# Performance work log

Hardware: AMD Instinct MI355X
Metric: run time of the kernel (lower is better)

The kernel has to match this reference:

```python
import jax, jax.numpy as jnp
import numpy as np

TEMPERATURE = 0.07
C_MARGIN = 0.5
T_MARGIN = 1.0
GAMMA = 2.0
ALPHA = 0.25
SMOOTHING = 0.1
W_CONTRASTIVE = 0.1
W_TRIPLET = 0.1
W_FOCAL = 0.4
W_LABEL_SMOOTH = 0.4


def setup_inputs() -> dict:
    key = jax.random.key(0)
    k1, k2, k3 = jax.random.split(key, 3)
    B, C, D = 2048, 1000, 512
    pred = jax.random.normal(k1, (B, C), dtype=jnp.float32)
    target = jax.random.randint(k2, (B,), 0, C, dtype=jnp.int64)
    features = jax.random.normal(k3, (B, D), dtype=jnp.float32)
    return {"pred": pred, "target": target, "features": features}


def _safe_cdist(f):
    # Euclidean pairwise distance with zero-grad at zero distance (matches torch.cdist on diagonal).
    r = jnp.sum(f * f, axis=1)
    d2 = jnp.maximum(r[:, None] - 2.0 * (f @ f.T) + r[None, :], 0.0)
    pos = d2 > 0
    return jnp.sqrt(jnp.where(pos, d2, 1.0)) * pos


def _contrastive(features, labels):
    f = features / jnp.linalg.norm(features, axis=1, keepdims=True)
    sim = f @ f.T  # [B, B]
    lm = (labels[:, None] == labels[None, :]).astype(sim.dtype)
    pos = sim * lm
    pos_loss = -jnp.log(jnp.exp(pos / TEMPERATURE) + 1e-8)
    neg = sim * (1.0 - lm)
    neg_loss = jnp.maximum(C_MARGIN - neg, 0.0)
    return pos_loss.mean() + neg_loss.mean()


def _triplet(features, labels):
    B = features.shape[0]
    d = _safe_cdist(features)  # [B, B]
    lm = (labels[:, None] == labels[None, :]).astype(d.dtype)
    pm, nm = lm, 1.0 - lm

    def body(acc, args):
        di, pmi, nmi = args  # [B], [B], [B]
        # sum over (p, n): relu(d_ip - d_in + margin), masked
        contrib = jnp.sum(
            jnp.maximum(di[:, None] - di[None, :] + T_MARGIN, 0.0)
            * pmi[:, None] * nmi[None, :]
        )
        return acc + contrib, None

    loss, _ = jax.lax.scan(body, jnp.float32(0.0), (d, pm, nm))
    return loss / (B + 1e-8)


def _focal(pred, target):
    logp = jax.nn.log_softmax(pred, axis=1)
    ce = -jnp.take_along_axis(logp, target[:, None], axis=1)[:, 0]
    pt = jnp.exp(-ce)
    return (ALPHA * (1.0 - pt) ** GAMMA * ce).mean()


def _label_smoothing(pred, target):
    C = pred.shape[1]
    off = SMOOTHING / (C - 1)
    logp = jax.nn.log_softmax(pred, axis=1)
    # smooth target: off everywhere, (1 - smoothing) at target index
    tgt_logp = jnp.take_along_axis(logp, target[:, None], axis=1)[:, 0]
    loss = -(off * logp.sum(axis=1) + ((1.0 - SMOOTHING) - off) * tgt_logp)
    return loss.mean()


def reference(pred, target, features):
    lc = _contrastive(features, target)
    lt = _triplet(features, target)
    lf = _focal(pred, target)
    ls = _label_smoothing(pred, target)
    total = (W_CONTRASTIVE * lc + W_TRIPLET * lt
             + W_FOCAL * lf + W_LABEL_SMOOTH * ls)
    return jnp.stack([lc, lt, lf, ls, total])
```

## Files before the change

### kernel.cpp

```cpp
#include <hip/hip_runtime.h>
#include <hip/hip_bf16.h>
#include <math.h>

typedef __attribute__((ext_vector_type(8))) short bf16x8;
typedef __attribute__((ext_vector_type(4))) float f32x4;

static constexpr float TEMP_INV  = 1.0f / 0.07f;
static constexpr float C_MARGIN  = 0.5f;
static constexpr float T_MARGIN  = 1.0f;
static constexpr float ALPHA     = 0.25f;
static constexpr float SMOOTHING = 0.1f;

__device__ __forceinline__ void gload_lds16(const void* g, void* l) {
    __builtin_amdgcn_global_load_lds(
        (const __attribute__((address_space(1))) void*)g,
        (__attribute__((address_space(3))) void*)l,
        16, 0, 0);
}

__device__ __forceinline__ unsigned short f2bf(float x) {
    __hip_bfloat16 h = __float2bfloat16(x);
    return *reinterpret_cast<unsigned short*>(&h);
}
__device__ __forceinline__ float bf2f(unsigned short u) {
    union { unsigned int u32; float f; } U;
    U.u32 = ((unsigned int)u) << 16;
    return U.f;
}

__global__ __launch_bounds__(256) void prep_kernel(
    const float* __restrict__ F, unsigned short* __restrict__ Fb,
    float* __restrict__ diag, float* __restrict__ inv_norm, int D) {
    const int row  = blockIdx.x * 4 + (threadIdx.x >> 6);
    const int lane = threadIdx.x & 63;
    const float4* Fr  = (const float4*)(F + (size_t)row * D);
    ushort4*      Fbr = (ushort4*)(Fb + (size_t)row * D);
    const int n4 = D >> 2;
    float s = 0.0f;
    for (int idx = lane; idx < n4; idx += 64) {
        float4 v = Fr[idx];
        s += v.x * v.x + v.y * v.y + v.z * v.z + v.w * v.w;
        ushort4 o;
        o.x = f2bf(v.x); o.y = f2bf(v.y); o.z = f2bf(v.z); o.w = f2bf(v.w);
        Fbr[idx] = o;
    }
#pragma unroll
    for (int off = 32; off > 0; off >>= 1) s += __shfl_down(s, off, 64);
    if (lane == 0) { diag[row] = s; inv_norm[row] = 1.0f / sqrtf(s); }
}

__global__ __launch_bounds__(256) void gram_ce_kernel(
    const unsigned short* __restrict__ Fb, unsigned short* __restrict__ Gb,
    const float* __restrict__ pred, const int* __restrict__ target,
    float* __restrict__ partialCE, int B, int D, int C, float off_const,
    int tilesX) {
    __shared__ unsigned short As[128 * 32];
    __shared__ unsigned short Bs[128 * 32];
    __shared__ float red[12];

    const int nTiles = tilesX * tilesX;
    const int tid = threadIdx.x;
    const int lane = tid & 63, wid = tid >> 6;

    if (blockIdx.x < nTiles) {
        const int rowBase = (blockIdx.x / tilesX) * 128;
        const int colBase = (blockIdx.x % tilesX) * 128;
        const int w = wid, l = lane;
        const int wr = (w >> 1) * 64;
        const int wc = (w & 1) * 64;
        const int half = l >> 4;
        const int rr   = l & 15;

        const unsigned short* FA = Fb + (size_t)rowBase * D;
        const unsigned short* FB = Fb + (size_t)colBase * D;

        f32x4 acc[4][4];
#pragma unroll
        for (int m = 0; m < 4; ++m)
#pragma unroll
            for (int n = 0; n < 4; ++n) acc[m][n] = (f32x4){0.f, 0.f, 0.f, 0.f};

        for (int k0 = 0; k0 < D; k0 += 32) {
#pragma unroll
            for (int c = 0; c < 2; ++c) {
                const int chunk = c * 256 + w * 64 + l;
                const int r2 = chunk >> 2;
                const int ss = (l & 3) ^ (r2 & 3);
                const size_t eoff = (size_t)r2 * D + k0 + ss * 8;
                gload_lds16(FA + eoff, &As[(c * 256 + w * 64) * 8]);
                gload_lds16(FB + eoff, &Bs[(c * 256 + w * 64) * 8]);
            }
            __syncthreads();
            bf16x8 af[4], bfv[4];
#pragma unroll
            for (int f = 0; f < 4; ++f) {
                const int ar = wr + f * 16 + rr;
                af[f]  = *(const bf16x8*)(&As[ar * 32 + ((half ^ (ar & 3)) * 8)]);
                const int br = wc + f * 16 + rr;
                bfv[f] = *(const bf16x8*)(&Bs[br * 32 + ((half ^ (br & 3)) * 8)]);
            }
#pragma unroll
            for (int m = 0; m < 4; ++m)
#pragma unroll
                for (int n = 0; n < 4; ++n)
                    acc[m][n] = __builtin_amdgcn_mfma_f32_16x16x32_bf16(
                        af[m], bfv[n], acc[m][n], 0, 0, 0);
            __syncthreads();
        }
#pragma unroll
        for (int m = 0; m < 4; ++m) {
            const int i0 = rowBase + wr + m * 16 + half * 4;
#pragma unroll
            for (int n = 0; n < 4; ++n) {
                const int j = colBase + wc + n * 16 + rr;
#pragma unroll
                for (int r = 0; r < 4; ++r)
                    Gb[(size_t)(i0 + r) * B + j] = f2bf(acc[m][n][r]);
            }
        }
    } else {
        const int i = blockIdx.x - nTiles;
        const float* prow = pred + (size_t)i * C;
        const float tlogit = prow[target[i]];
        const int Cv = C >> 2;

        float m = -1e30f, s = 0.0f, sp = 0.0f;
        for (int idx = tid; idx < Cv; idx += 256) {
            float4 v = ((const float4*)prow)[idx];
            float mv = fmaxf(fmaxf(v.x, v.y), fmaxf(v.z, v.w));
            if (mv > m) { s *= expf(m - mv); m = mv; }
            s += expf(v.x - m) + expf(v.y - m) + expf(v.z - m) + expf(v.w - m);
            sp += v.x + v.y + v.z + v.w;
        }
        for (int j = Cv * 4 + tid; j < C; j += 256) {
            float v = prow[j];
            if (v > m) { s *= expf(m - v); m = v; }
            s += expf(v - m);
            sp += v;
        }
#pragma unroll
        for (int off = 32; off > 0; off >>= 1) {
            float mo = __shfl_down(m, off, 64);
            float so = __shfl_down(s, off, 64);
            sp += __shfl_down(sp, off, 64);
            float mx = fmaxf(m, mo);
            s = s * expf(m - mx) + so * expf(mo - mx);
            m = mx;
        }
        if (lane == 0) { red[wid] = m; red[4 + wid] = s; red[8 + wid] = sp; }
        __syncthreads();
        if (tid == 0) {
            float mm = red[0], ss = red[4], spT = red[8];
#pragma unroll
            for (int q = 1; q < 4; ++q) {
                float mo = red[q], so = red[4 + q];
                float mn = fmaxf(mm, mo);
                ss = ss * expf(mm - mn) + so * expf(mo - mn);
                mm = mn;
                spT += red[8 + q];
            }
            float lse = mm + logf(ss);
            float tl  = tlogit - lse;
            float ce  = -tl;
            float pt  = expf(tl);
            float omp = 1.0f - pt;
            float focal = ALPHA * omp * omp * ce;
            float sumlogp = spT - (float)C * lse;
            float lsv = -(off_const * sumlogp + ((1.0f - SMOOTHING) - off_const) * tl);
            partialCE[(size_t)i * 2]     = focal;
            partialCE[(size_t)i * 2 + 1] = lsv;
        }
    }
}

__global__ __launch_bounds__(256) void row_loss_kernel(
    const unsigned short* __restrict__ Gb, const float* __restrict__ diag,
    const float* __restrict__ inv_norm, const int* __restrict__ labels,
    float* __restrict__ partial, int B) {
    __shared__ float p_d[256];
    __shared__ float red[12];
    __shared__ int p_cnt;
    const int tid = threadIdx.x;
    const int i = blockIdx.x;
    if (tid == 0) p_cnt = 0;
    __syncthreads();

    const int   li     = labels[i];
    const float ri     = diag[i];
    const float inv_ni = inv_norm[i];
    const int   j0     = tid * 8;

    union { uint4 u; unsigned short s[8]; } GV;
    GV.u = *(const uint4*)(Gb + (size_t)i * B + j0);
    int lab[8];
    *(int4*)&lab[0] = *(const int4*)(labels + j0);
    *(int4*)&lab[4] = *(const int4*)(labels + j0 + 4);
    float dg[8], ivn[8];
    *(float4*)&dg[0]  = *(const float4*)(diag + j0);
    *(float4*)&dg[4]  = *(const float4*)(diag + j0 + 4);
    *(float4*)&ivn[0] = *(const float4*)(inv_norm + j0);
    *(float4*)&ivn[4] = *(const float4*)(inv_norm + j0 + 4);

    float pos = 0.0f, neg = 0.0f;
    float d8[8];
    int mmask = 0;
#pragma unroll
    for (int e = 0; e < 8; ++e) {
        const int j = j0 + e;
        const float g = bf2f(GV.s[e]);
        float sim = g * inv_ni * ivn[e];
        const float d2 = ri - 2.0f * g + dg[e];
        float d = (d2 > 0.0f) ? sqrtf(d2) : 0.0f;
        if (j == i) { sim = 1.0f; d = 0.0f; }
        d8[e] = d;
        if (lab[e] == li) {
            pos += -logf(expf(sim * TEMP_INV) + 1e-8f);
            neg += C_MARGIN;
            mmask |= (1 << e);
            int slot = atomicAdd(&p_cnt, 1);
            if (slot < 256) p_d[slot] = d;
        } else {
            neg += fmaxf(C_MARGIN - sim, 0.0f);
        }
    }
    __syncthreads();
    const int cnt = (p_cnt < 256) ? p_cnt : 256;
    float trip = 0.0f;
    for (int p = 0; p < cnt; ++p) {
        const float dp = p_d[p] + T_MARGIN;
#pragma unroll
        for (int e = 0; e < 8; ++e)
            if (!(mmask & (1 << e))) trip += fmaxf(dp - d8[e], 0.0f);
    }

    float r0 = pos, r1 = neg, r2 = trip;
#pragma unroll
    for (int off = 32; off > 0; off >>= 1) {
        r0 += __shfl_down(r0, off, 64);
        r1 += __shfl_down(r1, off, 64);
        r2 += __shfl_down(r2, off, 64);
    }
    const int lane = tid & 63, wid = tid >> 6;
    if (lane == 0) { red[wid] = r0; red[4 + wid] = r1; red[8 + wid] = r2; }
    __syncthreads();
    if (tid == 0) {
        float4 o;
        o.x = red[0] + red[1] + red[2] + red[3];
        o.y = red[4] + red[5] + red[6] + red[7];
        o.z = red[8] + red[9] + red[10] + red[11];
        o.w = 0.0f;
        *(float4*)(partial + (size_t)i * 4) = o;
    }
}

__global__ __launch_bounds__(256) void reduce_kernel(
    const float* __restrict__ partialT, const float* __restrict__ partialCE,
    float* __restrict__ out, int B) {
    __shared__ float red[4][5];
    const int tid = threadIdx.x;
    float s[5] = {0.f, 0.f, 0.f, 0.f, 0.f};
    for (int r = tid; r < B; r += 256) {
        float4 v = *(const float4*)(partialT + (size_t)r * 4);
        s[0] += v.x; s[1] += v.y; s[2] += v.z;
    }
    for (int t = tid; t < (B * 2) / 4; t += 256) {
        float4 v = *(const float4*)(partialCE + (size_t)t * 4);
        s[3] += v.x + v.z; s[4] += v.y + v.w;
    }
#pragma unroll
    for (int off = 32; off > 0; off >>= 1) {
#pragma unroll
        for (int k = 0; k < 5; ++k) s[k] += __shfl_down(s[k], off, 64);
    }
    const int lane = tid & 63, wid = tid >> 6;
    if (lane == 0) {
#pragma unroll
        for (int k = 0; k < 5; ++k) red[wid][k] = s[k];
    }
    __syncthreads();
    if (tid == 0) {
        float t[5];
#pragma unroll
        for (int k = 0; k < 5; ++k)
            t[k] = red[0][k] + red[1][k] + red[2][k] + red[3][k];
        double invB2 = 1.0 / ((double)B * (double)B);
        float lc = (float)(((double)t[0] + (double)t[1]) * invB2);
        float lt = (float)((double)t[2] / ((double)B + 1e-8));
        float lf = t[3] / (float)B;
        float ls = t[4] / (float)B;
        out[0] = lc;
        out[1] = lt;
        out[2] = lf;
        out[3] = ls;
        out[4] = 0.1f * lc + 0.1f * lt + 0.4f * lf + 0.4f * ls;
    }
}

extern "C" void kernel_launch(void* const* d_in, const int* in_sizes, int n_in,
                              void* d_out, int out_size, void* d_ws, size_t ws_size,
                              hipStream_t stream) {
    const float* pred     = (const float*)d_in[0];
    const int*   target   = (const int*)d_in[1];
    const float* features = (const float*)d_in[2];
    const int B = in_sizes[1];
    const int C = in_sizes[0] / B;
    const int D = in_sizes[2] / B;
    float* out = (float*)d_out;
    const int tilesX = B / 128;
    const int nTiles = tilesX * tilesX;

    float* partial   = (float*)d_ws;
    float* partialCE = partial + (size_t)B * 4;
    float* diag      = partialCE + (size_t)B * 2;
    float* inv_norm  = diag + B;
    unsigned short* Fb = (unsigned short*)(inv_norm + B);
    unsigned short* Gb = Fb + (size_t)B * D;

    prep_kernel<<<B / 4, 256, 0, stream>>>(features, Fb, diag, inv_norm, D);

    float off_const = SMOOTHING / (float)(C - 1);
    gram_ce_kernel<<<nTiles + B, 256, 0, stream>>>(
        Fb, Gb, pred, target, partialCE, B, D, C, off_const, tilesX);

    row_loss_kernel<<<B, 256, 0, stream>>>(Gb, diag, inv_norm, target,
                                           partial, B);

    reduce_kernel<<<1, 256, 0, stream>>>(partial, partialCE, out, B);
}
```

Baseline: 38.15 us.

## Exploit Gram symmetry to compute upper tiles only; process several rows per block

The Gram kernel now computes only tiles on or above the diagonal and writes each off-diagonal tile twice, once as is and once transposed, which roughly halves the MFMA work. The row-loss kernel handles four rows per block and loads the per-column labels, norms and diag values once for all four. The transposed stores are strided 8-byte writes, which may coalesce poorly. Early-returning blocks still take launch slots.

Measured after the change: 44.39 us. 16.3% more time.

```diff
diff --git a/kernel.cpp b/kernel.cpp
--- a/kernel.cpp
+++ b/kernel.cpp
@@ -10,6 +10,7 @@
 static constexpr float T_MARGIN  = 1.0f;
 static constexpr float ALPHA     = 0.25f;
 static constexpr float SMOOTHING = 0.1f;
+static constexpr int   RPB       = 4;
 
 __device__ __forceinline__ void gload_lds16(const void* g, void* l) {
     __builtin_amdgcn_global_load_lds(
@@ -63,8 +64,11 @@
     const int lane = tid & 63, wid = tid >> 6;
 
     if (blockIdx.x < nTiles) {
-        const int rowBase = (blockIdx.x / tilesX) * 128;
-        const int colBase = (blockIdx.x % tilesX) * 128;
+        const int ti = blockIdx.x / tilesX;
+        const int tj = blockIdx.x % tilesX;
+        if (tj < ti) return;
+        const int rowBase = ti * 128;
+        const int colBase = tj * 128;
         const int w = wid, l = lane;
         const int wr = (w >> 1) * 64;
         const int wc = (w & 1) * 64;
@@ -116,6 +120,22 @@
 #pragma unroll
                 for (int r = 0; r < 4; ++r)
                     Gb[(size_t)(i0 + r) * B + j] = f2bf(acc[m][n][r]);
+            }
+        }
+        if (ti != tj) {
+#pragma unroll
+            for (int m = 0; m < 4; ++m) {
+                const int i0 = rowBase + wr + m * 16 + half * 4;
+#pragma unroll
+                for (int n = 0; n < 4; ++n) {
+                    const int gj = colBase + wc + n * 16 + rr;
+                    ushort4 tw;
+                    tw.x = f2bf(acc[m][n][0]);
+                    tw.y = f2bf(acc[m][n][1]);
+                    tw.z = f2bf(acc[m][n][2]);
+                    tw.w = f2bf(acc[m][n][3]);
+                    *(ushort4*)(Gb + (size_t)gj * B + i0) = tw;
+                }
             }
         }
     } else {
@@ -181,17 +201,9 @@
     __shared__ float red[12];
     __shared__ int p_cnt;
     const int tid = threadIdx.x;
-    const int i = blockIdx.x;
-    if (tid == 0) p_cnt = 0;
-    __syncthreads();
-
-    const int   li     = labels[i];
-    const float ri     = diag[i];
-    const float inv_ni = inv_norm[i];
-    const int   j0     = tid * 8;
-
-    union { uint4 u; unsigned short s[8]; } GV;
-    GV.u = *(const uint4*)(Gb + (size_t)i * B + j0);
+    const int lane = tid & 63, wid = tid >> 6;
+    const int j0 = tid * 8;
+
     int lab[8];
     *(int4*)&lab[0] = *(const int4*)(labels + j0);
     *(int4*)&lab[4] = *(const int4*)(labels + j0 + 4);
@@ -201,55 +213,68 @@
     *(float4*)&ivn[0] = *(const float4*)(inv_norm + j0);
     *(float4*)&ivn[4] = *(const float4*)(inv_norm + j0 + 4);
 
-    float pos = 0.0f, neg = 0.0f;
-    float d8[8];
-    int mmask = 0;
-#pragma unroll
-    for (int e = 0; e < 8; ++e) {
-        const int j = j0 + e;
-        const float g = bf2f(GV.s[e]);
-        float sim = g * inv_ni * ivn[e];
-        const float d2 = ri - 2.0f * g + dg[e];
-        float d = (d2 > 0.0f) ? sqrtf(d2) : 0.0f;
-        if (j == i) { sim = 1.0f; d = 0.0f; }
-        d8[e] = d;
-        if (lab[e] == li) {
-            pos += -logf(expf(sim * TEMP_INV) + 1e-8f);
-            neg += C_MARGIN;
-            mmask |= (1 << e);
-            int slot = atomicAdd(&p_cnt, 1);
-            if (slot < 256) p_d[slot] = d;
-        } else {
-            neg += fmaxf(C_MARGIN - sim, 0.0f);
-        }
-    }
-    __syncthreads();
-    const int cnt = (p_cnt < 256) ? p_cnt : 256;
-    float trip = 0.0f;
-    for (int p = 0; p < cnt; ++p) {
-        const float dp = p_d[p] + T_MARGIN;
-#pragma unroll
-        for (int e = 0; e < 8; ++e)
-            if (!(mmask & (1 << e))) trip += fmaxf(dp - d8[e], 0.0f);
-    }
-
-    float r0 = pos, r1 = neg, r2 = trip;
-#pragma unroll
-    for (int off = 32; off > 0; off >>= 1) {
-        r0 += __shfl_down(r0, off, 64);
-        r1 += __shfl_down(r1, off, 64);
-        r2 += __shfl_down(r2, off, 64);
-    }
-    const int lane = tid & 63, wid = tid >> 6;
-    if (lane == 0) { red[wid] = r0; red[4 + wid] = r1; red[8 + wid] = r2; }
-    __syncthreads();
-    if (tid == 0) {
-        float4 o;
-        o.x = red[0] + red[1] + red[2] + red[3];
-        o.y = red[4] + red[5] + red[6] + red[7];
-        o.z = red[8] + red[9] + red[10] + red[11];
-        o.w = 0.0f;
-        *(float4*)(partial + (size_t)i * 4) = o;
+    const int iBase = blockIdx.x * RPB;
+    for (int ir = 0; ir < RPB; ++ir) {
+        const int i = iBase + ir;
+        if (tid == 0) p_cnt = 0;
+        __syncthreads();
+
+        const int   li     = labels[i];
+        const float ri     = diag[i];
+        const float inv_ni = inv_norm[i];
+
+        union { uint4 u; unsigned short s[8]; } GV;
+        GV.u = *(const uint4*)(Gb + (size_t)i * B + j0);
+
+        float pos = 0.0f, neg = 0.0f;
+        float d8[8];
+        int mmask = 0;
+#pragma unroll
+        for (int e = 0; e < 8; ++e) {
+            const int j = j0 + e;
+            const float g = bf2f(GV.s[e]);
+            float sim = g * inv_ni * ivn[e];
+            const float d2 = ri - 2.0f * g + dg[e];
+            float d = (d2 > 0.0f) ? sqrtf(d2) : 0.0f;
+            if (j == i) { sim = 1.0f; d = 0.0f; }
+            d8[e] = d;
+            if (lab[e] == li) {
+                pos += -logf(expf(sim * TEMP_INV) + 1e-8f);
+                neg += C_MARGIN;
+                mmask |= (1 << e);
+                int slot = atomicAdd(&p_cnt, 1);
+                if (slot < 256) p_d[slot] = d;
+            } else {
+                neg += fmaxf(C_MARGIN - sim, 0.0f);
+            }
+        }
+        __syncthreads();
+        const int cnt = (p_cnt < 256) ? p_cnt : 256;
+        float trip = 0.0f;
+        for (int p = 0; p < cnt; ++p) {
+            const float dp = p_d[p] + T_MARGIN;
+#pragma unroll
+            for (int e = 0; e < 8; ++e)
+                if (!(mmask & (1 << e))) trip += fmaxf(dp - d8[e], 0.0f);
+        }
+
+        float r0 = pos, r1 = neg, r2 = trip;
+#pragma unroll
+        for (int off = 32; off > 0; off >>= 1) {
+            r0 += __shfl_down(r0, off, 64);
+            r1 += __shfl_down(r1, off, 64);
+            r2 += __shfl_down(r2, off, 64);
+        }
+        if (lane == 0) { red[wid] = r0; red[4 + wid] = r1; red[8 + wid] = r2; }
+        __syncthreads();
+        if (tid == 0) {
+            float4 o;
+            o.x = red[0] + red[1] + red[2] + red[3];
+            o.y = red[4] + red[5] + red[6] + red[7];
+            o.z = red[8] + red[9] + red[10] + red[11];
+            o.w = 0.0f;
+            *(float4*)(partial + (size_t)i * 4) = o;
+        }
     }
 }
 
@@ -322,8 +347,8 @@
     gram_ce_kernel<<<nTiles + B, 256, 0, stream>>>(
         Fb, Gb, pred, target, partialCE, B, D, C, off_const, tilesX);
 
-    row_loss_kernel<<<B, 256, 0, stream>>>(Gb, diag, inv_norm, target,
-                                           partial, B);
+    row_loss_kernel<<<B / RPB, 256, 0, stream>>>(Gb, diag, inv_norm, target,
+                                                 partial, B);
 
     reduce_kernel<<<1, 256, 0, stream>>>(partial, partialCE, out, B);
 }
```
